# Kernel optimization log

Hardware: AMD Instinct MI355X
Metric: run time of the kernel (lower is better)

The kernel has to match this reference:

```python
import math
import jax, jax.numpy as jnp
import numpy as np
from jax import lax

MUL_IN, MUL_OUT = 8, 16
DIM_IN, DIM_OUT = 4 * MUL_IN, 4 * MUL_OUT  # 0e(1) + 1o(3) per multiplicity
DIAMETER = 3.0
STEPS = (1.0, 1.0, 1.0)
NUM_RB = 4
BATCH, GRID = 8, 32


def _lattice():
    r = DIAMETER / 2
    axes = [np.arange(-math.floor(r / s), math.floor(r / s) + 1.0) * s for s in STEPS]
    return jnp.asarray(np.stack(np.meshgrid(*axes, indexing='ij'), axis=-1), jnp.float32)  # [X,Y,Z,3]


def _sus(x):
    # smooth unit step: exp(-1/x) for x>0 else 0
    return jnp.where(x > 0.0, jnp.exp(-1.0 / jnp.where(x > 0.0, x, 1.0)), 0.0)


def _radial_emb(lattice):
    # soft_one_hot_linspace, basis='smooth_finite', cutoff=True
    dist = jnp.linalg.norm(lattice, axis=-1)
    values = jnp.linspace(0.0, DIAMETER / 2, NUM_RB + 2)
    step = values[1] - values[0]
    diff = (dist[..., None] - values[1:-1]) / step
    return 1.14136 * jnp.exp(2.0) * _sus(diff + 1.0) * _sus(1.0 - diff)  # [X,Y,Z,NUM_RB]


def _sph(lattice):
    # real spherical harmonics l=0,1; normalize=True, 'component' normalization
    norm = jnp.linalg.norm(lattice, axis=-1, keepdims=True)
    unit = lattice / jnp.where(norm == 0.0, 1.0, norm)
    sh0 = jnp.ones(lattice.shape[:-1] + (1,), lattice.dtype)
    sh1 = jnp.sqrt(jnp.float32(3.0)) * unit
    return sh0, sh1


def setup_inputs() -> dict:
    key = jax.random.key(0)
    ks = jax.random.split(key, 7)
    x = jax.random.normal(ks[0], (BATCH, GRID, GRID, GRID, DIM_IN), jnp.float32)
    w_lin0 = jax.random.normal(ks[1], (MUL_IN, MUL_OUT), jnp.float32)
    w_lin1 = jax.random.normal(ks[2], (MUL_IN, MUL_OUT), jnp.float32)
    pshape = (NUM_RB, MUL_IN, 1, MUL_OUT)
    w000 = jax.random.normal(ks[3], pshape, jnp.float32)
    w011 = jax.random.normal(ks[4], pshape, jnp.float32)
    w101 = jax.random.normal(ks[5], pshape, jnp.float32)
    w110 = jax.random.normal(ks[6], pshape, jnp.float32)
    return dict(x=x, w_lin0=w_lin0, w_lin1=w_lin1, w000=w000, w011=w011, w101=w101, w110=w110)


def _forward(x, w_lin0, w_lin1, w000, w011, w101, w110):
    lattice = _lattice()
    emb = _radial_emb(lattice)
    sh0, sh1 = _sph(lattice)
    n_lat = lattice.shape[0] * lattice.shape[1] * lattice.shape[2]

    # ---- self-connection: FunctionalLinear(irreps_in -> irreps_out), per-l blocks ----
    lin_norm = 1.0 / math.sqrt(MUL_IN)
    x0 = x[..., :MUL_IN]                                             # [B,X,Y,Z,8]
    x1 = x[..., MUL_IN:].reshape(x.shape[:-1] + (MUL_IN, 3))         # [B,X,Y,Z,8,3]
    sc0 = jnp.einsum('...u,uw->...w', x0, w_lin0) * lin_norm
    sc1 = (jnp.einsum('...ui,uw->...wi', x1, w_lin1) * lin_norm).reshape(x.shape[:-1] + (3 * MUL_OUT,))
    sc = jnp.concatenate([sc0, sc1], axis=-1)                        # [B,X,Y,Z,DIM_OUT]

    # ---- radial weights per lattice point: einsum('xyzk,k...->xyz...') / n_lat ----
    def rad(w):
        return jnp.einsum('xyzk,kuvw->xyzuw', emb, w) / n_lat        # sh mul v == 1 squeezed
    r000, r011, r101, r110 = rad(w000), rad(w011), rad(w101), rad(w110)

    # ---- CG tensor-product 'right': build kernel [X,Y,Z, DIM_IN, DIM_OUT] ----
    inv_s3 = 1.0 / math.sqrt(3.0)  # w3j(0,1,1)=w3j(1,0,1)=w3j(1,1,0)=eye/sqrt(3); w3j(0,0,0)=1
    alpha = 1.0 / math.sqrt(2.0 * MUL_IN)  # 2 paths feed each output irrep, fan mul_in each

    eye3 = jnp.eye(3, dtype=x.dtype)
    # in 0e x sh 0e -> out 0e
    k00 = alpha * r000 * sh0[..., 0][..., None, None]                 # [X,Y,Z,8,16]
    # in 0e x sh 1o -> out 1o
    k01 = (alpha * inv_s3) * jnp.einsum('xyzuw,xyzm->xyzuwm', r011, sh1)
    k01 = k01.reshape(k01.shape[:3] + (MUL_IN, 3 * MUL_OUT))          # [X,Y,Z,8,48]
    # in 1o x sh 1o -> out 0e
    k10 = (alpha * inv_s3) * jnp.einsum('xyzuw,xyzi->xyzuiw', r110, sh1)
    k10 = k10.reshape(k10.shape[:3] + (3 * MUL_IN, MUL_OUT))          # [X,Y,Z,24,16]
    # in 1o x sh 0e -> out 1o
    k11 = (alpha * inv_s3) * jnp.einsum('xyzuw,im->xyzuiwm', r101 * sh0[..., 0][..., None, None], eye3)
    k11 = k11.reshape(k11.shape[:3] + (3 * MUL_IN, 3 * MUL_OUT))      # [X,Y,Z,24,48]

    k = jnp.concatenate([
        jnp.concatenate([k00, k01], axis=-1),
        jnp.concatenate([k10, k11], axis=-1),
    ], axis=-2)                                                       # [X,Y,Z,DIM_IN,DIM_OUT]

    conv = lax.conv_general_dilated(
        lhs=x, rhs=k, window_strides=(1, 1, 1), padding='SAME',
        dimension_numbers=('NXYZC', 'XYZIO', 'NXYZC'))
    return sc + conv


def reference(x, w_lin0, w_lin1, w000, w011, w101, w110):
    return _forward(x, w_lin0, w_lin1, w000, w011, w101, w110)
```

## Files before the change

kernel.cpp:

```cpp
#include <hip/hip_runtime.h>


typedef __attribute__((ext_vector_type(8))) short bf16x8;
typedef __attribute__((ext_vector_type(4))) float f32x4;
typedef unsigned int u32;

__device__ __forceinline__ float sus_f(float v) { return v > 0.f ? __expf(-1.f / v) : 0.f; }

__device__ __forceinline__ unsigned short f2bf(float f) {
    union { float f; unsigned u; } c; c.f = f;
    unsigned u = c.u;
    u += 0x7FFFu + ((u >> 16) & 1u);
    return (unsigned short)(u >> 16);
}

__global__ __launch_bounds__(256) void prep_all(
    const float* __restrict__ x,
    const float* __restrict__ w_lin0, const float* __restrict__ w_lin1,
    const float* __restrict__ w000,  const float* __restrict__ w011,
    const float* __restrict__ w101,  const float* __restrict__ w110,
    unsigned short* __restrict__ xb, unsigned short* __restrict__ kw,
    int koff)
{
    const int bid = blockIdx.x;
    const int tid = threadIdx.x;

    if (bid < koff) {
        const int gi = bid * 256 + tid;
        const int vox = gi >> 2, g = gi & 3;
        const int gz = vox & 31;
        const float4* sp = reinterpret_cast<const float4*>(x) + (size_t)gi * 2;
        const float4 lo = sp[0], hi = sp[1];
        bf16x8 w;
        w[0] = (short)f2bf(lo.x); w[1] = (short)f2bf(lo.y);
        w[2] = (short)f2bf(lo.z); w[3] = (short)f2bf(lo.w);
        w[4] = (short)f2bf(hi.x); w[5] = (short)f2bf(hi.y);
        w[6] = (short)f2bf(hi.z); w[7] = (short)f2bf(hi.w);
        const int slot = g ^ (((gz + 1) >> 1) & 3);
        const size_t dst = ((size_t)(vox >> 5) << 10) + (gz << 5) + (slot << 3);
        *reinterpret_cast<bf16x8*>(xb + dst) = w;
        return;
    }

    const int taps[19] = {1,3,4,5,7,9,10,11,12,13,14,15,16,17,19,21,22,23,25};
    const int ta = bid - koff;
    const int t = taps[ta];
    const int a = t / 9, b = (t / 3) % 3, c = t % 3;

    const float fx = (float)(a - 1), fy = (float)(b - 1), fz = (float)(c - 1);
    const float dist = sqrtf(fx * fx + fy * fy + fz * fz);
    float emb[4];
    #pragma unroll
    for (int r = 0; r < 4; ++r) {
        const float v = 0.3f * (float)(r + 1);
        const float d = (dist - v) * (1.0f / 0.3f);
        emb[r] = 8.4335731f * sus_f(d + 1.f) * sus_f(1.f - d);
    }
    const float s = (dist > 0.f) ? (1.7320508f / dist) : 0.f;
    const float shv[3] = { fx * s, fy * s, fz * s };
    const float S000 = 0.25f / 27.f;
    const float S1   = 0.25f * 0.57735027f / 27.f;
    const float LNRM = 0.35355339f;

    const int ci = tid >> 3;
    #pragma unroll
    for (int j = 0; j < 8; ++j) {
        const int o = (tid & 7) * 8 + j;
        float val;
        if (ci < 8) {
            const int u = ci;
            if (o < 16) {
                const float* p = w000 + u * 16 + o;
                val = S000 * (emb[0]*p[0] + emb[1]*p[128] + emb[2]*p[256] + emb[3]*p[384]);
                if (t == 13) val += LNRM * w_lin0[u * 16 + o];
            } else {
                const int oo = o - 16, w = oo / 3, m = oo % 3;
                const float* p = w011 + u * 16 + w;
                val = S1 * shv[m] * (emb[0]*p[0] + emb[1]*p[128] + emb[2]*p[256] + emb[3]*p[384]);
            }
        } else {
            const int iu = ci - 8, u = iu / 3, ic = iu % 3;
            if (o < 16) {
                const float* p = w110 + u * 16 + o;
                val = S1 * shv[ic] * (emb[0]*p[0] + emb[1]*p[128] + emb[2]*p[256] + emb[3]*p[384]);
            } else {
                const int oo = o - 16, w = oo / 3, m = oo % 3;
                if (ic == m) {
                    const float* p = w101 + u * 16 + w;
                    val = S1 * (emb[0]*p[0] + emb[1]*p[128] + emb[2]*p[256] + emb[3]*p[384]);
                    if (t == 13) val += LNRM * w_lin1[u * 16 + w];
                } else {
                    val = 0.f;
                }
            }
        }
        const int g = ci >> 3, slot = ci & 7, nt = o >> 4, cc = o & 15;
        const int lane = (g << 4) | cc;
        kw[((size_t)(ta * 4 + nt) * 64 + lane) * 8 + slot] = f2bf(val);
    }
}

template<bool DIRECT>
__global__ __launch_bounds__(256, 2) void conv_mfma(
    const float* __restrict__ x,
    const unsigned short* __restrict__ xb,
    const unsigned short* __restrict__ kw,
    float* __restrict__ out)
{
    __shared__ unsigned short lx[3 * 10 * 34 * 32];

    const int tid = threadIdx.x;
    const int bid = blockIdx.x;
    const int xcd = bid & 7, idx = bid >> 3;
    const int gid = xcd * 128 + idx;
    const int n = gid >> 7, X = (gid >> 2) & 31, Yg = gid & 3;
    const int Y0 = Yg * 8;
    const int wid = tid >> 6, l = tid & 63, lr = l & 15, lg = l >> 4;

    const bf16x8* kwf = reinterpret_cast<const bf16x8*>(kw);

    bf16x8 bring[4][4];
    #pragma unroll
    for (int p = 0; p < 3; ++p)
        #pragma unroll
        for (int nt = 0; nt < 4; ++nt)
            bring[p][nt] = kwf[(size_t)(p * 4 + nt) * 64 + l];

    if (tid < 60) {
        const int row = tid >> 1, zp = (tid & 1) * 33;
        f32x4* dp = reinterpret_cast<f32x4*>(
            reinterpret_cast<char*>(lx) + row * 2176 + zp * 64);
        #pragma unroll
        for (int q = 0; q < 4; ++q) dp[q] = (f32x4)0.f;
    }

    if (DIRECT) {
        #pragma unroll
        for (int k = 0; k < 8; ++k) {
            const int rr = wid + (k << 2);
            if (rr < 30) {
                const int dx = rr / 10, y6 = rr - dx * 10;
                const int gx = X + dx - 1, gy = Y0 + y6 - 1;
                char* dstrow = reinterpret_cast<char*>(lx) + rr * 2176 + 64;
                if ((unsigned)gx < 32u && (unsigned)gy < 32u) {
                    const char* src = reinterpret_cast<const char*>(xb) +
                        ((size_t)((n * 32 + gx) * 32 + gy) << 11);
                    __builtin_amdgcn_global_load_lds(
                        (const __attribute__((address_space(1))) u32*)(src + l * 16),
                        (__attribute__((address_space(3))) u32*)(dstrow), 16, 0, 0);
                    __builtin_amdgcn_global_load_lds(
                        (const __attribute__((address_space(1))) u32*)(src + 1024 + l * 16),
                        (__attribute__((address_space(3))) u32*)(dstrow + 1024), 16, 0, 0);
                } else {
                    bf16x8 zz = (bf16x8)(short)0;
                    *reinterpret_cast<bf16x8*>(dstrow + l * 16) = zz;
                    *reinterpret_cast<bf16x8*>(dstrow + 1024 + l * 16) = zz;
                }
            }
        }
    } else {
        for (int it = tid; it < 960; it += 256) {
            const int dx = it / 320, rem = it - dx * 320;
            const int y6 = rem >> 5, z = rem & 31;
            const int gx = X + dx - 1, gy = Y0 + y6 - 1;
            char* row = reinterpret_cast<char*>(lx) + (dx * 10 + y6) * 2176 + (z + 1) * 64;
            if ((unsigned)gx < 32u && (unsigned)gy < 32u) {
                const float4* sp = reinterpret_cast<const float4*>(
                    x + ((size_t)(((n * 32 + gx) * 32 + gy) * 32 + z) << 5));
                const int swz = ((z + 1) >> 1) & 3;
                #pragma unroll
                for (int g = 0; g < 4; ++g) {
                    const float4 lo = sp[2 * g], hi = sp[2 * g + 1];
                    bf16x8 w;
                    w[0] = (short)f2bf(lo.x); w[1] = (short)f2bf(lo.y);
                    w[2] = (short)f2bf(lo.z); w[3] = (short)f2bf(lo.w);
                    w[4] = (short)f2bf(hi.x); w[5] = (short)f2bf(hi.y);
                    w[6] = (short)f2bf(hi.z); w[7] = (short)f2bf(hi.w);
                    *reinterpret_cast<bf16x8*>(row + ((g ^ swz) << 4)) = w;
                }
            } else {
                bf16x8 zz = (bf16x8)(short)0;
                #pragma unroll
                for (int g = 0; g < 4; ++g)
                    *reinterpret_cast<bf16x8*>(row + (g << 4)) = zz;
            }
        }
    }
    __syncthreads();

    constexpr int TA[19] = {1,3,4,5,7,9,10,11,12,13,14,15,16,17,19,21,22,23,25};
    const char* lxc = reinterpret_cast<const char*>(lx);
    const int yloc = wid * 2;

    f32x4 acc[4][4];
    #pragma unroll
    for (int r = 0; r < 4; ++r)
        #pragma unroll
        for (int nt = 0; nt < 4; ++nt) acc[r][nt] = (f32x4)0.f;

    #pragma unroll
    for (int ta = 0; ta < 19; ++ta) {
        const int t = TA[ta];
        const int a = t / 9, b = (t / 3) % 3, c = t % 3;

        if (ta + 3 < 19) {
            #pragma unroll
            for (int nt = 0; nt < 4; ++nt)
                bring[(ta + 3) & 3][nt] = kwf[(size_t)((ta + 3) * 4 + nt) * 64 + l];
        }

        bf16x8 af[4];
        #pragma unroll
        for (int r = 0; r < 4; ++r) {
            const int y10 = yloc + (r >> 1) + b;
            const int zp = 16 * (r & 1) + lr + c;
            const int byte = ((a * 10 + y10) * 34 + zp) * 64 + ((lg ^ ((zp >> 1) & 3)) << 4);
            af[r] = *reinterpret_cast<const bf16x8*>(lxc + byte);
        }

        #pragma unroll
        for (int r = 0; r < 4; ++r)
            #pragma unroll
            for (int nt = 0; nt < 4; ++nt)
                acc[r][nt] = __builtin_amdgcn_mfma_f32_16x16x32_bf16(
                    af[r], bring[ta & 3][nt], acc[r][nt], 0, 0, 0);
    }

    float* ob = out + ((size_t)(((n * 32 + X) * 32 + Y0 + yloc) * 32) << 6);
    #pragma unroll
    for (int r = 0; r < 4; ++r) {
        float* oy = ob + (size_t)(r >> 1) * 2048;
        #pragma unroll
        for (int nt = 0; nt < 4; ++nt)
            #pragma unroll
            for (int reg = 0; reg < 4; ++reg) {
                const int z = 16 * (r & 1) + 4 * lg + reg;
                oy[z * 64 + nt * 16 + lr] = acc[r][nt][reg];
            }
    }
}

extern "C" void kernel_launch(void* const* d_in, const int* in_sizes, int n_in,
                              void* d_out, int out_size, void* d_ws, size_t ws_size,
                              hipStream_t stream) {
    const float* x    = (const float*)d_in[0];
    const float* wl0  = (const float*)d_in[1];
    const float* wl1  = (const float*)d_in[2];
    const float* w000 = (const float*)d_in[3];
    const float* w011 = (const float*)d_in[4];
    const float* w101 = (const float*)d_in[5];
    const float* w110 = (const float*)d_in[6];
    float* out = (float*)d_out;

    unsigned short* kw = (unsigned short*)d_ws;
    const size_t KWB = 77824;
    const size_t XBB = 16777216ull;

    if (ws_size >= KWB + XBB) {
        unsigned short* xb = (unsigned short*)((char*)d_ws + KWB);
        prep_all<<<dim3(4096 + 19), dim3(256), 0, stream>>>(
            x, wl0, wl1, w000, w011, w101, w110, xb, kw, 4096);
        conv_mfma<true><<<dim3(1024), dim3(256), 0, stream>>>(x, xb, kw, out);
    } else {
        prep_all<<<dim3(19), dim3(256), 0, stream>>>(
            x, wl0, wl1, w000, w011, w101, w110, nullptr, kw, 0);
        conv_mfma<false><<<dim3(1024), dim3(256), 0, stream>>>(x, nullptr, kw, out);
    }
}
```

Before: 42.51 us.

## Walk two X-planes per block with rotating three-plane LDS buffer

Each conv block now computes two consecutive X output planes, keeping a rotating set of three staged input planes in LDS so the shared planes are loaded once instead of twice. The fourth plane is prefetched into the freed slot after the first taps finish, overlapping the load with the remaining MFMA work. The grid is halved to 512 blocks and the block-to-XCD mapping changes to batch-major. This cuts redundant global-to-LDS traffic but reduces parallelism and adds extra barriers.

```diff
diff --git a/kernel.cpp b/kernel.cpp
--- a/kernel.cpp
+++ b/kernel.cpp
@@ -4,6 +4,8 @@
 typedef __attribute__((ext_vector_type(8))) short bf16x8;
 typedef __attribute__((ext_vector_type(4))) float f32x4;
 typedef unsigned int u32;
+
+__device__ constexpr int TAt[19] = {1,3,4,5,7,9,10,11,12,13,14,15,16,17,19,21,22,23,25};
 
 __device__ __forceinline__ float sus_f(float v) { return v > 0.f ? __expf(-1.f / v) : 0.f; }
 
@@ -42,9 +44,8 @@
         return;
     }
 
-    const int taps[19] = {1,3,4,5,7,9,10,11,12,13,14,15,16,17,19,21,22,23,25};
     const int ta = bid - koff;
-    const int t = taps[ta];
+    const int t = TAt[ta];
     const int a = t / 9, b = (t / 3) % 3, c = t % 3;
 
     const float fx = (float)(a - 1), fy = (float)(b - 1), fz = (float)(c - 1);
@@ -100,9 +101,41 @@
     }
 }
 
-template<bool DIRECT>
-__global__ __launch_bounds__(256, 2) void conv_mfma(
-    const float* __restrict__ x,
+template<int LO, int HI>
+__device__ __forceinline__ void tap_range(
+    const char* lxc, const bf16x8* kwf, int l, int lr, int lg, int yloc,
+    int s0, int s1, int s2, bf16x8 (&bring)[4][4], f32x4 (&acc)[4][4])
+{
+    #pragma unroll
+    for (int ta = LO; ta < HI; ++ta) {
+        const int t = TAt[ta];
+        const int a = t / 9, b = (t / 3) % 3, c = t % 3;
+
+        if (ta + 3 < 19) {
+            #pragma unroll
+            for (int nt = 0; nt < 4; ++nt)
+                bring[(ta + 3) & 3][nt] = kwf[(size_t)((ta + 3) * 4 + nt) * 64 + l];
+        }
+
+        const int sbase = (a == 0 ? s0 : (a == 1 ? s1 : s2)) * 21760;
+        bf16x8 af[4];
+        #pragma unroll
+        for (int r = 0; r < 4; ++r) {
+            const int y10 = yloc + (r >> 1) + b;
+            const int zp = 16 * (r & 1) + lr + c;
+            af[r] = *reinterpret_cast<const bf16x8*>(
+                lxc + sbase + (y10 * 34 + zp) * 64 + ((lg ^ ((zp >> 1) & 3)) << 4));
+        }
+        #pragma unroll
+        for (int r = 0; r < 4; ++r)
+            #pragma unroll
+            for (int nt = 0; nt < 4; ++nt)
+                acc[r][nt] = __builtin_amdgcn_mfma_f32_16x16x32_bf16(
+                    af[r], bring[ta & 3][nt], acc[r][nt], 0, 0, 0);
+    }
+}
+
+__global__ __launch_bounds__(256, 2) void conv_walk2(
     const unsigned short* __restrict__ xb,
     const unsigned short* __restrict__ kw,
     float* __restrict__ out)
@@ -111,40 +144,36 @@
 
     const int tid = threadIdx.x;
     const int bid = blockIdx.x;
-    const int xcd = bid & 7, idx = bid >> 3;
-    const int gid = xcd * 128 + idx;
-    const int n = gid >> 7, X = (gid >> 2) & 31, Yg = gid & 3;
+    const int n = bid & 7;
+    const int idx = bid >> 3;
+    const int Xc = idx >> 2, Yg = idx & 3;
+    const int X0 = Xc * 2;
     const int Y0 = Yg * 8;
     const int wid = tid >> 6, l = tid & 63, lr = l & 15, lg = l >> 4;
+    const int yloc = wid * 2;
 
     const bf16x8* kwf = reinterpret_cast<const bf16x8*>(kw);
+    char* lxc = reinterpret_cast<char*>(lx);
 
     bf16x8 bring[4][4];
-    #pragma unroll
-    for (int p = 0; p < 3; ++p)
-        #pragma unroll
-        for (int nt = 0; nt < 4; ++nt)
-            bring[p][nt] = kwf[(size_t)(p * 4 + nt) * 64 + l];
-
-    if (tid < 60) {
-        const int row = tid >> 1, zp = (tid & 1) * 33;
-        f32x4* dp = reinterpret_cast<f32x4*>(
-            reinterpret_cast<char*>(lx) + row * 2176 + zp * 64);
-        #pragma unroll
-        for (int q = 0; q < 4; ++q) dp[q] = (f32x4)0.f;
-    }
-
-    if (DIRECT) {
-        #pragma unroll
-        for (int k = 0; k < 8; ++k) {
+    auto ring_preload = [&]() {
+        #pragma unroll
+        for (int p = 0; p < 3; ++p)
+            #pragma unroll
+            for (int nt = 0; nt < 4; ++nt)
+                bring[p][nt] = kwf[(size_t)(p * 4 + nt) * 64 + l];
+    };
+
+    auto stage_direct = [&](int p, int s) {
+        #pragma unroll
+        for (int k = 0; k < 3; ++k) {
             const int rr = wid + (k << 2);
-            if (rr < 30) {
-                const int dx = rr / 10, y6 = rr - dx * 10;
-                const int gx = X + dx - 1, gy = Y0 + y6 - 1;
-                char* dstrow = reinterpret_cast<char*>(lx) + rr * 2176 + 64;
-                if ((unsigned)gx < 32u && (unsigned)gy < 32u) {
+            if (rr < 10) {
+                const int gy = Y0 + rr - 1;
+                char* dstrow = lxc + s * 21760 + rr * 2176 + 64;
+                if ((unsigned)p < 32u && (unsigned)gy < 32u) {
                     const char* src = reinterpret_cast<const char*>(xb) +
-                        ((size_t)((n * 32 + gx) * 32 + gy) << 11);
+                        ((size_t)((n * 32 + p) * 32 + gy) << 11);
                     __builtin_amdgcn_global_load_lds(
                         (const __attribute__((address_space(1))) u32*)(src + l * 16),
                         (__attribute__((address_space(3))) u32*)(dstrow), 16, 0, 0);
@@ -158,37 +187,123 @@
                 }
             }
         }
-    } else {
-        for (int it = tid; it < 960; it += 256) {
-            const int dx = it / 320, rem = it - dx * 320;
-            const int y6 = rem >> 5, z = rem & 31;
-            const int gx = X + dx - 1, gy = Y0 + y6 - 1;
-            char* row = reinterpret_cast<char*>(lx) + (dx * 10 + y6) * 2176 + (z + 1) * 64;
-            if ((unsigned)gx < 32u && (unsigned)gy < 32u) {
-                const float4* sp = reinterpret_cast<const float4*>(
-                    x + ((size_t)(((n * 32 + gx) * 32 + gy) * 32 + z) << 5));
-                const int swz = ((z + 1) >> 1) & 3;
+    };
+
+    auto epilogue = [&](int X, f32x4 (&acc)[4][4]) {
+        float* ob = out + ((size_t)(((n * 32 + X) * 32 + Y0 + yloc) * 32) << 6);
+        #pragma unroll
+        for (int r = 0; r < 4; ++r) {
+            float* oy = ob + (size_t)(r >> 1) * 2048;
+            #pragma unroll
+            for (int nt = 0; nt < 4; ++nt)
                 #pragma unroll
-                for (int g = 0; g < 4; ++g) {
-                    const float4 lo = sp[2 * g], hi = sp[2 * g + 1];
-                    bf16x8 w;
-                    w[0] = (short)f2bf(lo.x); w[1] = (short)f2bf(lo.y);
-                    w[2] = (short)f2bf(lo.z); w[3] = (short)f2bf(lo.w);
-                    w[4] = (short)f2bf(hi.x); w[5] = (short)f2bf(hi.y);
-                    w[6] = (short)f2bf(hi.z); w[7] = (short)f2bf(hi.w);
-                    *reinterpret_cast<bf16x8*>(row + ((g ^ swz) << 4)) = w;
+                for (int reg = 0; reg < 4; ++reg) {
+                    const int z = 16 * (r & 1) + 4 * lg + reg;
+                    oy[z * 64 + nt * 16 + lr] = acc[r][nt][reg];
                 }
-            } else {
-                bf16x8 zz = (bf16x8)(short)0;
-                #pragma unroll
-                for (int g = 0; g < 4; ++g)
-                    *reinterpret_cast<bf16x8*>(row + (g << 4)) = zz;
-            }
-        }
-    }
+        }
+    };
+
+    const int sm = (X0 + 2) % 3;
+    const int s0 = X0 % 3;
+    const int s1 = (X0 + 1) % 3;
+
+    ring_preload();
+    if (tid < 60) {
+        const int s = tid / 20, rem = tid % 20;
+        const int rr = rem >> 1, zp = (rem & 1) * 33;
+        f32x4* dp = reinterpret_cast<f32x4*>(lxc + s * 21760 + rr * 2176 + zp * 64);
+        #pragma unroll
+        for (int q = 0; q < 4; ++q) dp[q] = (f32x4)0.f;
+    }
+    stage_direct(X0 - 1, sm);
+    stage_direct(X0,     s0);
+    stage_direct(X0 + 1, s1);
     __syncthreads();
 
-    constexpr int TA[19] = {1,3,4,5,7,9,10,11,12,13,14,15,16,17,19,21,22,23,25};
+    f32x4 acc[4][4];
+    #pragma unroll
+    for (int r = 0; r < 4; ++r)
+        #pragma unroll
+        for (int nt = 0; nt < 4; ++nt) acc[r][nt] = (f32x4)0.f;
+
+    tap_range<0, 5>(lxc, kwf, l, lr, lg, yloc, sm, s0, s1, bring, acc);
+    __syncthreads();
+    stage_direct(X0 + 2, sm);
+    tap_range<5, 19>(lxc, kwf, l, lr, lg, yloc, sm, s0, s1, bring, acc);
+    ring_preload();
+    epilogue(X0, acc);
+    __syncthreads();
+
+    #pragma unroll
+    for (int r = 0; r < 4; ++r)
+        #pragma unroll
+        for (int nt = 0; nt < 4; ++nt) acc[r][nt] = (f32x4)0.f;
+
+    tap_range<0, 19>(lxc, kwf, l, lr, lg, yloc, s0, s1, sm, bring, acc);
+    epilogue(X0 + 1, acc);
+}
+
+__global__ __launch_bounds__(256, 2) void conv_fb(
+    const float* __restrict__ x,
+    const unsigned short* __restrict__ kw,
+    float* __restrict__ out)
+{
+    __shared__ unsigned short lx[3 * 10 * 34 * 32];
+
+    const int tid = threadIdx.x;
+    const int bid = blockIdx.x;
+    const int xcd = bid & 7, idx = bid >> 3;
+    const int gid = xcd * 128 + idx;
+    const int n = gid >> 7, X = (gid >> 2) & 31, Yg = gid & 3;
+    const int Y0 = Yg * 8;
+    const int wid = tid >> 6, l = tid & 63, lr = l & 15, lg = l >> 4;
+
+    const bf16x8* kwf = reinterpret_cast<const bf16x8*>(kw);
+
+    bf16x8 bring[4][4];
+    #pragma unroll
+    for (int p = 0; p < 3; ++p)
+        #pragma unroll
+        for (int nt = 0; nt < 4; ++nt)
+            bring[p][nt] = kwf[(size_t)(p * 4 + nt) * 64 + l];
+
+    if (tid < 60) {
+        const int row = tid >> 1, zp = (tid & 1) * 33;
+        f32x4* dp = reinterpret_cast<f32x4*>(
+            reinterpret_cast<char*>(lx) + row * 2176 + zp * 64);
+        #pragma unroll
+        for (int q = 0; q < 4; ++q) dp[q] = (f32x4)0.f;
+    }
+
+    for (int it = tid; it < 960; it += 256) {
+        const int dx = it / 320, rem = it - dx * 320;
+        const int y6 = rem >> 5, z = rem & 31;
+        const int gx = X + dx - 1, gy = Y0 + y6 - 1;
+        char* row = reinterpret_cast<char*>(lx) + (dx * 10 + y6) * 2176 + (z + 1) * 64;
+        if ((unsigned)gx < 32u && (unsigned)gy < 32u) {
+            const float4* sp = reinterpret_cast<const float4*>(
+                x + ((size_t)(((n * 32 + gx) * 32 + gy) * 32 + z) << 5));
+            const int swz = ((z + 1) >> 1) & 3;
+            #pragma unroll
+            for (int g = 0; g < 4; ++g) {
+                const float4 lo = sp[2 * g], hi = sp[2 * g + 1];
+                bf16x8 w;
+                w[0] = (short)f2bf(lo.x); w[1] = (short)f2bf(lo.y);
+                w[2] = (short)f2bf(lo.z); w[3] = (short)f2bf(lo.w);
+                w[4] = (short)f2bf(hi.x); w[5] = (short)f2bf(hi.y);
+                w[6] = (short)f2bf(hi.z); w[7] = (short)f2bf(hi.w);
+                *reinterpret_cast<bf16x8*>(row + ((g ^ swz) << 4)) = w;
+            }
+        } else {
+            bf16x8 zz = (bf16x8)(short)0;
+            #pragma unroll
+            for (int g = 0; g < 4; ++g)
+                *reinterpret_cast<bf16x8*>(row + (g << 4)) = zz;
+        }
+    }
+    __syncthreads();
+
     const char* lxc = reinterpret_cast<const char*>(lx);
     const int yloc = wid * 2;
 
@@ -198,33 +313,7 @@
         #pragma unroll
         for (int nt = 0; nt < 4; ++nt) acc[r][nt] = (f32x4)0.f;
 
-    #pragma unroll
-    for (int ta = 0; ta < 19; ++ta) {
-        const int t = TA[ta];
-        const int a = t / 9, b = (t / 3) % 3, c = t % 3;
-
-        if (ta + 3 < 19) {
-            #pragma unroll
-            for (int nt = 0; nt < 4; ++nt)
-                bring[(ta + 3) & 3][nt] = kwf[(size_t)((ta + 3) * 4 + nt) * 64 + l];
-        }
-
-        bf16x8 af[4];
-        #pragma unroll
-        for (int r = 0; r < 4; ++r) {
-            const int y10 = yloc + (r >> 1) + b;
-            const int zp = 16 * (r & 1) + lr + c;
-            const int byte = ((a * 10 + y10) * 34 + zp) * 64 + ((lg ^ ((zp >> 1) & 3)) << 4);
-            af[r] = *reinterpret_cast<const bf16x8*>(lxc + byte);
-        }
-
-        #pragma unroll
-        for (int r = 0; r < 4; ++r)
-            #pragma unroll
-            for (int nt = 0; nt < 4; ++nt)
-                acc[r][nt] = __builtin_amdgcn_mfma_f32_16x16x32_bf16(
-                    af[r], bring[ta & 3][nt], acc[r][nt], 0, 0, 0);
-    }
+    tap_range<0, 19>(lxc, kwf, l, lr, lg, yloc, 0, 1, 2, bring, acc);
 
     float* ob = out + ((size_t)(((n * 32 + X) * 32 + Y0 + yloc) * 32) << 6);
     #pragma unroll
@@ -260,10 +349,10 @@
         unsigned short* xb = (unsigned short*)((char*)d_ws + KWB);
         prep_all<<<dim3(4096 + 19), dim3(256), 0, stream>>>(
             x, wl0, wl1, w000, w011, w101, w110, xb, kw, 4096);
-        conv_mfma<true><<<dim3(1024), dim3(256), 0, stream>>>(x, xb, kw, out);
+        conv_walk2<<<dim3(512), dim3(256), 0, stream>>>(xb, kw, out);
     } else {
         prep_all<<<dim3(19), dim3(256), 0, stream>>>(
             x, wl0, wl1, w000, w011, w101, w110, nullptr, kw, 0);
-        conv_mfma<false><<<dim3(1024), dim3(256), 0, stream>>>(x, nullptr, kw, out);
-    }
-}
+        conv_fb<<<dim3(1024), dim3(256), 0, stream>>>(x, kw, out);
+    }
+}
```

Result: slower. 49.80 us (+17.2%).
